# Kernel tuning notes

Measured on AMD Instinct MI355X. Metric: run time of the kernel, lower is better.

The kernel has to match this reference:

```python
import jax, jax.numpy as jnp
import numpy as np

KERNEL = 25  # moving_avg


def _series_decomp_trend(x, kernel):
    # x: [B, L, N]; replicate-pad ends then moving average over time (AvgPool1d stride 1)
    pad = (kernel - 1) // 2
    front = jnp.repeat(x[:, :1, :], pad, axis=1)
    end = jnp.repeat(x[:, -1:, :], pad, axis=1)
    xp = jnp.concatenate([front, x, end], axis=1)  # [B, L+2*pad, N]
    cs = jnp.cumsum(xp, axis=1)
    cs = jnp.concatenate([jnp.zeros_like(cs[:, :1, :]), cs], axis=1)
    trend = (cs[:, kernel:, :] - cs[:, :-kernel, :]) / kernel  # [B, L, N]
    return trend


def setup_inputs() -> dict:
    key = jax.random.key(0)
    k1, k2, k3 = jax.random.split(key, 3)
    B, L, N = 128, 512, 321
    x_enc = jax.random.normal(k1, (B, L, N), dtype=jnp.float32)
    W_trend = jax.random.normal(k2, (L, L), dtype=jnp.float32) * (1.0 / L)
    b_trend = jax.random.normal(k3, (L,), dtype=jnp.float32) * 0.02
    return {"x_enc": x_enc, "W_trend": W_trend, "b_trend": b_trend}


def reference(x_enc, W_trend, b_trend):
    B, L, N = x_enc.shape
    # series_decomp: only the trend branch is consumed downstream
    trend = _series_decomp_trend(x_enc, KERNEL)          # [B, L, N]
    trend_init = trend.transpose(0, 2, 1)                # [B, N, L]
    # Linear_Trend: seq_len -> pred_len (== L)
    trend_out = jnp.einsum('bnl,pl->bnp', trend_init, W_trend) + b_trend  # [B, N, L]
    # closed-form OLS per (b, n): X_b = [1, t] for t in [-L, 0)
    t_old = jnp.arange(-L, 0, dtype=jnp.float32)
    t_new = jnp.arange(L, dtype=jnp.float32)
    X_b = jnp.stack([jnp.ones(L, jnp.float32), t_old], axis=1)      # [L, 2]
    X_new_b = jnp.stack([jnp.ones(L, jnp.float32), t_new], axis=1)  # [L, 2]
    XTX = X_b.T @ X_b                                    # [2, 2]
    XTy = jnp.einsum('lt,bnl->bnt', X_b, trend_out)      # [B, N, 2]
    inv = jnp.linalg.inv(XTX)                            # symmetric 2x2
    theta = jnp.einsum('bnt,ts->bns', XTy, inv)          # [B, N, 2]
    pred = jnp.einsum('pt,bnt->bnp', X_new_b, theta)     # [B, N, L]
    out = pred.transpose(0, 2, 1)                        # [B, L, N]
    return out[:, -L:, :]  # pred_len == L, so this is the full output
```

## Files before the change

### kernel.cpp

```cpp
#include <hip/hip_runtime.h>

#define LSEQ 512
#define NCH  321
#define BATCH 128
#define KAVG 25
#define PAD  12
#define NB1A 64
#define ROWS1A 8

constexpr double S1d  = -131328.0;
constexpr double S2d  = 44870400.0;
constexpr double DETD = 512.0 * S2d - S1d * S1d;
constexpr double I00  = S2d / DETD;
constexpr double I01  = -S1d / DETD;
constexpr double I11  = 512.0 / DETD;

__global__ __launch_bounds__(512) void colsum_kernel(const float* __restrict__ W,
                                                     float* __restrict__ part0,
                                                     float* __restrict__ part1) {
    int l = threadIdx.x;
    int p0 = blockIdx.x * ROWS1A;
    double s0 = 0.0, s1 = 0.0;
#pragma unroll
    for (int r = 0; r < ROWS1A; ++r) {
        float w = W[(p0 + r) * LSEQ + l];
        s0 += (double)w;
        s1 += (double)(p0 + r - LSEQ) * (double)w;
    }
    part0[blockIdx.x * LSEQ + l] = (float)s0;
    part1[blockIdx.x * LSEQ + l] = (float)s1;
}

__global__ __launch_bounds__(512) void prep_kernel(const float* __restrict__ part0,
                                                   const float* __restrict__ part1,
                                                   const float* __restrict__ bvec,
                                                   float* __restrict__ alpha,
                                                   float* __restrict__ beta,
                                                   float* __restrict__ consts) {
    __shared__ double w0d[LSEQ], w1d[LSEQ];
    __shared__ double r0[LSEQ], r1[LSEQ];
    int l = threadIdx.x;
    double s0 = 0.0, s1 = 0.0;
    for (int j = 0; j < NB1A; ++j) {
        s0 += (double)part0[j * LSEQ + l];
        s1 += (double)part1[j * LSEQ + l];
    }
    w0d[l] = s0;
    w1d[l] = s1;
    double bv = (double)bvec[l];
    r0[l] = bv;
    r1[l] = (double)(l - LSEQ) * bv;
    __syncthreads();

    double g0 = 0.0, g1 = 0.0;
    for (int m = l - PAD; m <= l + PAD; ++m) {
        if (m >= 0 && m < LSEQ) { g0 += w0d[m]; g1 += w1d[m]; }
    }
    if (l == 0) {
        for (int m = 0; m < PAD; ++m) {
            double c = (double)(PAD - m);
            g0 += c * w0d[m]; g1 += c * w1d[m];
        }
    }
    if (l == LSEQ - 1) {
        for (int m = LSEQ - PAD; m < LSEQ; ++m) {
            double c = (double)(m - (LSEQ - PAD - 1));
            g0 += c * w0d[m]; g1 += c * w1d[m];
        }
    }
    g0 *= (1.0 / (double)KAVG);
    g1 *= (1.0 / (double)KAVG);
    alpha[l] = (float)(I00 * g0 + I01 * g1);
    beta[l]  = (float)(I01 * g0 + I11 * g1);

    for (int s = LSEQ / 2; s > 0; s >>= 1) {
        __syncthreads();
        if (l < s) { r0[l] += r0[l + s]; r1[l] += r1[l + s]; }
    }
    if (l == 0) {
        consts[0] = (float)(I00 * r0[0] + I01 * r1[0]);
        consts[1] = (float)(I01 * r0[0] + I11 * r1[0]);
    }
}

__global__ __launch_bounds__(256) void main_kernel(const float* __restrict__ x,
                                                   const float* __restrict__ alpha,
                                                   const float* __restrict__ beta,
                                                   const float* __restrict__ consts,
                                                   float* __restrict__ out) {
    __shared__ float la[LSEQ], lbb[LSEQ];
    __shared__ float pa[4][64], pb[4][64];
    int tid = threadIdx.x;
    la[tid]        = alpha[tid];
    la[tid + 256]  = alpha[tid + 256];
    lbb[tid]       = beta[tid];
    lbb[tid + 256] = beta[tid + 256];
    float ca = consts[0];
    float cb = consts[1];
    __syncthreads();

    int wave = tid >> 6;
    int lane = tid & 63;
    int n = blockIdx.x * 64 + lane;
    bool valid = (n < NCH);
    int b = blockIdx.y;
    int base = b * (LSEQ * NCH) + n;
    int l0 = wave * 128;

    float a0 = 0.f, a1 = 0.f, a2 = 0.f, a3 = 0.f;
    float b0 = 0.f, b1 = 0.f, b2 = 0.f, b3 = 0.f;
    if (valid) {
        const float* xp = x + base;
#pragma unroll 8
        for (int i = 0; i < 128; i += 4) {
            int l = l0 + i;
            float v0 = xp[(l + 0) * NCH];
            float v1 = xp[(l + 1) * NCH];
            float v2 = xp[(l + 2) * NCH];
            float v3 = xp[(l + 3) * NCH];
            a0 = fmaf(v0, la[l + 0], a0);  b0 = fmaf(v0, lbb[l + 0], b0);
            a1 = fmaf(v1, la[l + 1], a1);  b1 = fmaf(v1, lbb[l + 1], b1);
            a2 = fmaf(v2, la[l + 2], a2);  b2 = fmaf(v2, lbb[l + 2], b2);
            a3 = fmaf(v3, la[l + 3], a3);  b3 = fmaf(v3, lbb[l + 3], b3);
        }
    }
    pa[wave][lane] = (a0 + a1) + (a2 + a3);
    pb[wave][lane] = (b0 + b1) + (b2 + b3);
    __syncthreads();

    float th0 = ((pa[0][lane] + pa[1][lane]) + (pa[2][lane] + pa[3][lane])) + ca;
    float th1 = ((pb[0][lane] + pb[1][lane]) + (pb[2][lane] + pb[3][lane])) + cb;

    if (valid) {
        float* op = out + base;
#pragma unroll 8
        for (int p = l0; p < l0 + 128; ++p) {
            op[p * NCH] = fmaf((float)p, th1, th0);
        }
    }
}

extern "C" void kernel_launch(void* const* d_in, const int* in_sizes, int n_in,
                              void* d_out, int out_size, void* d_ws, size_t ws_size,
                              hipStream_t stream) {
    (void)in_sizes; (void)n_in; (void)out_size; (void)ws_size;
    const float* x    = (const float*)d_in[0];
    const float* W    = (const float*)d_in[1];
    const float* bvec = (const float*)d_in[2];
    float* out = (float*)d_out;

    float* p0     = (float*)d_ws;
    float* p1     = p0 + NB1A * LSEQ;
    float* alpha  = p1 + NB1A * LSEQ;
    float* beta   = alpha + LSEQ;
    float* consts = beta + LSEQ;

    colsum_kernel<<<NB1A, LSEQ, 0, stream>>>(W, p0, p1);
    prep_kernel<<<1, LSEQ, 0, stream>>>(p0, p1, bvec, alpha, beta, consts);
    main_kernel<<<dim3((NCH + 63) / 64, BATCH), 256, 0, stream>>>(x, alpha, beta, consts, out);
}
```

Baseline: 51.70 us.

## Split main kernel into reduction and vectorized float4 write kernels

```diff
diff --git a/kernel.cpp b/kernel.cpp
--- a/kernel.cpp
+++ b/kernel.cpp
@@ -5,8 +5,8 @@
 #define BATCH 128
 #define KAVG 25
 #define PAD  12
-#define NB1A 64
-#define ROWS1A 8
+#define NB1A 32
+#define ROWS1A 16
 
 constexpr double S1d  = -131328.0;
 constexpr double S2d  = 44870400.0;
@@ -83,20 +83,17 @@
     }
 }
 
-__global__ __launch_bounds__(256) void main_kernel(const float* __restrict__ x,
-                                                   const float* __restrict__ alpha,
-                                                   const float* __restrict__ beta,
-                                                   const float* __restrict__ consts,
-                                                   float* __restrict__ out) {
+__global__ __launch_bounds__(512) void reduce_kernel(const float* __restrict__ x,
+                                                     const float* __restrict__ alpha,
+                                                     const float* __restrict__ beta,
+                                                     const float* __restrict__ consts,
+                                                     float* __restrict__ T0,
+                                                     float* __restrict__ T1) {
     __shared__ float la[LSEQ], lbb[LSEQ];
-    __shared__ float pa[4][64], pb[4][64];
+    __shared__ float pa[8][64], pb[8][64];
     int tid = threadIdx.x;
-    la[tid]        = alpha[tid];
-    la[tid + 256]  = alpha[tid + 256];
-    lbb[tid]       = beta[tid];
-    lbb[tid + 256] = beta[tid + 256];
-    float ca = consts[0];
-    float cb = consts[1];
+    la[tid]  = alpha[tid];
+    lbb[tid] = beta[tid];
     __syncthreads();
 
     int wave = tid >> 6;
@@ -104,15 +101,14 @@
     int n = blockIdx.x * 64 + lane;
     bool valid = (n < NCH);
     int b = blockIdx.y;
-    int base = b * (LSEQ * NCH) + n;
-    int l0 = wave * 128;
+    int l0 = wave * 64;
 
     float a0 = 0.f, a1 = 0.f, a2 = 0.f, a3 = 0.f;
     float b0 = 0.f, b1 = 0.f, b2 = 0.f, b3 = 0.f;
     if (valid) {
-        const float* xp = x + base;
-#pragma unroll 8
-        for (int i = 0; i < 128; i += 4) {
+        const float* xp = x + (size_t)b * (LSEQ * NCH) + n;
+#pragma unroll
+        for (int i = 0; i < 64; i += 4) {
             int l = l0 + i;
             float v0 = xp[(l + 0) * NCH];
             float v1 = xp[(l + 1) * NCH];
@@ -128,14 +124,45 @@
     pb[wave][lane] = (b0 + b1) + (b2 + b3);
     __syncthreads();
 
-    float th0 = ((pa[0][lane] + pa[1][lane]) + (pa[2][lane] + pa[3][lane])) + ca;
-    float th1 = ((pb[0][lane] + pb[1][lane]) + (pb[2][lane] + pb[3][lane])) + cb;
+    if (tid < 64 && valid) {
+        float s0 = 0.f, s1 = 0.f;
+#pragma unroll
+        for (int w = 0; w < 8; ++w) { s0 += pa[w][tid]; s1 += pb[w][tid]; }
+        T0[b * NCH + n] = s0 + consts[0];
+        T1[b * NCH + n] = s1 + consts[1];
+    }
+}
 
-    if (valid) {
-        float* op = out + base;
-#pragma unroll 8
-        for (int p = l0; p < l0 + 128; ++p) {
-            op[p * NCH] = fmaf((float)p, th1, th0);
+#define ROWS_W 8
+#define CHUNK (ROWS_W * NCH)
+__global__ __launch_bounds__(256) void write_kernel(const float* __restrict__ T0,
+                                                    const float* __restrict__ T1,
+                                                    float* __restrict__ out) {
+    __shared__ float t0s[NCH], t1s[NCH];
+    int tid = threadIdx.x;
+    int b = blockIdx.y;
+    for (int i = tid; i < NCH; i += 256) {
+        t0s[i] = T0[b * NCH + i];
+        t1s[i] = T1[b * NCH + i];
+    }
+    __syncthreads();
+
+    int pbase = blockIdx.x * ROWS_W;
+    float* op = out + (size_t)b * (LSEQ * NCH) + (size_t)pbase * NCH;
+#pragma unroll
+    for (int k = 0; k < 3; ++k) {
+        int g = tid + k * 256;
+        if (g < CHUNK / 4) {
+            int c0 = 4 * g;
+            int ploc = c0 / NCH;
+            int n = c0 - ploc * NCH;
+            float pf = (float)(pbase + ploc);
+            float4 v;
+            v.x = fmaf(pf, t1s[n], t0s[n]); if (++n == NCH) { n = 0; pf += 1.f; }
+            v.y = fmaf(pf, t1s[n], t0s[n]); if (++n == NCH) { n = 0; pf += 1.f; }
+            v.z = fmaf(pf, t1s[n], t0s[n]); if (++n == NCH) { n = 0; pf += 1.f; }
+            v.w = fmaf(pf, t1s[n], t0s[n]);
+            *reinterpret_cast<float4*>(op + c0) = v;
         }
     }
 }
@@ -149,13 +176,17 @@
     const float* bvec = (const float*)d_in[2];
     float* out = (float*)d_out;
 
-    float* p0     = (float*)d_ws;
-    float* p1     = p0 + NB1A * LSEQ;
-    float* alpha  = p1 + NB1A * LSEQ;
+    float* alpha  = (float*)d_ws;
     float* beta   = alpha + LSEQ;
     float* consts = beta + LSEQ;
+    float* region = consts + 2;
+    float* p0 = region;
+    float* p1 = p0 + NB1A * LSEQ;
+    float* T0 = region;
+    float* T1 = T0 + BATCH * NCH;
 
     colsum_kernel<<<NB1A, LSEQ, 0, stream>>>(W, p0, p1);
     prep_kernel<<<1, LSEQ, 0, stream>>>(p0, p1, bvec, alpha, beta, consts);
-    main_kernel<<<dim3((NCH + 63) / 64, BATCH), 256, 0, stream>>>(x, alpha, beta, consts, out);
+    reduce_kernel<<<dim3((NCH + 63) / 64, BATCH), 512, 0, stream>>>(x, alpha, beta, consts, T0, T1);
+    write_kernel<<<dim3(LSEQ / ROWS_W, BATCH), 256, 0, stream>>>(T0, T1, out);
 }
```

Measured after the change: 50.53 us. 1.02x faster.
